# Performance work log

Hardware: AMD Instinct MI355X
Metric: run time of the kernel (lower is better)

The kernel has to match this reference:

```python
import jax, jax.numpy as jnp
import numpy as np

B, S, D, H = 4, 4096, 1024, 8
HD = D // H  # head dims, FFT length for circular convolution


def setup_inputs() -> dict:
    key = jax.random.key(0)
    k1, k2, k3 = jax.random.split(key, 3)
    x = jax.random.normal(k1, (B, S, D), dtype=jnp.float32)
    # torch nn.Linear(D, 3D, bias=False) -> store as [D, 3D] for x @ W
    w_qkv = jax.random.normal(k2, (D, 3 * D), dtype=jnp.float32) * (1.0 / np.sqrt(D))
    w_out = jax.random.normal(k3, (D, D), dtype=jnp.float32) * (1.0 / np.sqrt(D))
    return {"x": x, "w_qkv": w_qkv, "w_out": w_out}


def reference(x, w_qkv, w_out):
    # HRR self-attention (causal, norm=False, dropout in eval mode => identity).
    b, s, d = x.shape
    qkv = x @ w_qkv                               # [B,S,3D]
    q, k, v = jnp.split(qkv, 3, axis=-1)
    q = q.reshape(b, s, H, HD)
    k = k.reshape(b, s, H, HD)
    v = v.reshape(b, s, H, HD)
    # Holographic binding: circular convolution k (*) v == ifft(fft(k)*fft(v))
    fq = jnp.fft.fft(q, axis=-1)                  # [B,S,H,HD] complex
    fk = jnp.fft.fft(k, axis=-1)
    fv = jnp.fft.fft(v, axis=-1)
    kv = fk * fv                                  # bound key-value pairs (freq domain)
    kv = jnp.cumsum(kv, axis=1)                   # causal aggregation over sequence
    # Unbinding via circular correlation with the query: ifft(S * conj(fft(q)))
    vals = jnp.fft.ifft(kv * jnp.conj(fq), axis=-1).real.astype(x.dtype)
    vals = vals.reshape(b, s, d)
    return vals @ w_out
```

## Files before the change

### kernel.cpp

```cpp
#include <hip/hip_runtime.h>

static constexpr int BB = 4;
static constexpr int SS = 4096;
static constexpr int DD = 1024;
static constexpr int HH = 8;
static constexpr int HD = 128;
static constexpr int CS = 32;
static constexpr int NCHUNK = SS / CS;
static constexpr int MROWS = BB * SS;

typedef __attribute__((ext_vector_type(8))) short bfrag;
typedef __attribute__((ext_vector_type(4))) float floatx4;

__device__ __forceinline__ float bf2f(unsigned int u) {
    return __uint_as_float((u & 0xFFFFu) << 16);
}
__device__ __forceinline__ unsigned short f2bf(float f) {
    unsigned int x = __float_as_uint(f);
    unsigned int r = x + 0x7FFFu + ((x >> 16) & 1u);
    return (unsigned short)(r >> 16);
}
__device__ __forceinline__ unsigned int pack_rne(float a, float b) {
    return ((unsigned int)f2bf(a)) | (((unsigned int)f2bf(b)) << 16);
}

__device__ __forceinline__ void async_copy16(const void* g, void* l) {
    __builtin_amdgcn_global_load_lds(
        (const __attribute__((address_space(1))) unsigned int*)g,
        (__attribute__((address_space(3))) unsigned int*)l, 16, 0, 0);
}

struct cpx { float re, im; };

__device__ __forceinline__ cpx cadd(cpx a, cpx b) { return {a.re + b.re, a.im + b.im}; }
__device__ __forceinline__ cpx csub(cpx a, cpx b) { return {a.re - b.re, a.im - b.im}; }
__device__ __forceinline__ cpx cmul(cpx a, cpx b) {
    return { fmaf(a.re, b.re, -a.im * b.im), fmaf(a.re, b.im, a.im * b.re) };
}
__device__ __forceinline__ cpx cmul_cj(cpx a, cpx b) {
    return { fmaf(a.re, b.re, a.im * b.im), fmaf(a.im, b.re, -a.re * b.im) };
}
__device__ __forceinline__ cpx shflx(cpx x, int m) {
    return { __shfl_xor(x.re, m), __shfl_xor(x.im, m) };
}
__device__ __forceinline__ cpx shfl_at(cpx x, int src) {
    return { __shfl(x.re, src), __shfl(x.im, src) };
}

__device__ __forceinline__ int pair_lane_even(int l) {
    int m = (int)(__brev((unsigned)l) >> 26);
    int mp = (64 - m) & 63;
    return (int)(__brev((unsigned)mp) >> 26);
}

__device__ __forceinline__ void make_tw(int lane, cpx tw[7]) {
    const float NEG2PI = -6.28318530717958647692f;
    float a0 = NEG2PI * (float)lane * (1.0f / 128.0f);
    tw[0] = { __cosf(a0), __sinf(a0) };
    int d = 32;
#pragma unroll
    for (int s = 1; s <= 6; ++s) {
        int i = lane & (d - 1);
        float a = NEG2PI * (float)i / (float)(2 * d);
        tw[s] = { __cosf(a), __sinf(a) };
        d >>= 1;
    }
}

__device__ __forceinline__ void fft128_fwd(cpx& x0, cpx& x1, const cpx tw[7], int lane) {
    cpx a = x0, b = x1;
    x0 = cadd(a, b);
    x1 = cmul(csub(a, b), tw[0]);
    int d = 32;
#pragma unroll
    for (int s = 1; s <= 6; ++s) {
        const bool up = (lane & d) != 0;
        cpx o0 = shflx(x0, d);
        cpx o1 = shflx(x1, d);
        cpx s0 = cadd(x0, o0);
        cpx s1 = cadd(x1, o1);
        cpx d0 = cmul(csub(o0, x0), tw[s]);
        cpx d1 = cmul(csub(o1, x1), tw[s]);
        x0 = up ? d0 : s0;
        x1 = up ? d1 : s1;
        d >>= 1;
    }
}

__device__ __forceinline__ void fft128_inv(cpx& x0, cpx& x1, const cpx tw[7], int lane) {
    int d = 1;
#pragma unroll
    for (int s = 6; s >= 1; --s) {
        const bool up = (lane & d) != 0;
        cpx o0 = shflx(x0, d);
        cpx o1 = shflx(x1, d);
        cpx b0 = up ? x0 : o0;
        cpx a0 = up ? o0 : x0;
        cpx b1 = up ? x1 : o1;
        cpx a1 = up ? o1 : x1;
        cpx t0 = cmul_cj(b0, tw[s]);
        cpx t1 = cmul_cj(b1, tw[s]);
        x0 = up ? csub(a0, t0) : cadd(a0, t0);
        x1 = up ? csub(a1, t1) : cadd(a1, t1);
        d <<= 1;
    }
    cpx t = cmul_cj(x1, tw[0]);
    cpx a = x0;
    const float inv = 0.0078125f;
    x0 = { (a.re + t.re) * inv, (a.im + t.im) * inv };
    x1 = { (a.re - t.re) * inv, (a.im - t.im) * inv };
}

__global__ __launch_bounds__(256) void convert_bf16(const float* __restrict__ X,
                                                    unsigned short* __restrict__ Y)
{
    const size_t i = ((size_t)blockIdx.x * 256 + threadIdx.x) * 8;
    float4 v0 = *reinterpret_cast<const float4*>(X + i);
    float4 v1 = *reinterpret_cast<const float4*>(X + i + 4);
    uint4 p = { pack_rne(v0.x, v0.y), pack_rne(v0.z, v0.w),
                pack_rne(v1.x, v1.y), pack_rne(v1.z, v1.w) };
    *reinterpret_cast<uint4*>(Y + i) = p;
}

__global__ __launch_bounds__(256) void transpose_rn(const float* __restrict__ W,
                                                    unsigned short* __restrict__ T,
                                                    int K, int N)
{
    __shared__ float tile[32][33];
    const int n0 = blockIdx.x * 32, k0 = blockIdx.y * 32;
    const int r = threadIdx.x >> 5, c = threadIdx.x & 31;
#pragma unroll
    for (int i = 0; i < 4; ++i)
        tile[r + 8 * i][c] = W[(size_t)(k0 + r + 8 * i) * N + n0 + c];
    __syncthreads();
#pragma unroll
    for (int i = 0; i < 4; ++i) {
        float v = tile[c][r + 8 * i];
        T[(size_t)(n0 + r + 8 * i) * K + k0 + c] = f2bf(v);
    }
}

template <typename OutT>
__global__ __launch_bounds__(512, 2) void gemm256(const unsigned short* __restrict__ A,
                                                  const unsigned short* __restrict__ Bt,
                                                  OutT* __restrict__ C,
                                                  int M, int N, int K)
{
    extern __shared__ __align__(16) unsigned short lds[];
    unsigned short* sA = lds;
    unsigned short* sB = lds + 32768;

    const int tid = threadIdx.x, lane = tid & 63, w = tid >> 6;
    const int wr = w >> 2, wc = w & 3;

    const int nbx = N >> 8;
    const int cpx_ = gridDim.x >> 3;
    const int wg = blockIdx.x;
    const int swz = (wg & 7) * cpx_ + (wg >> 3);
    const int n0 = (swz % nbx) << 8;
    const int m0 = (swz / nbx) << 8;

    const int lr = lane >> 2;
    const int kx = (((lane & 3) ^ ((lane >> 3) & 3)) << 3);
    const unsigned short* pA0 = A  + (size_t)(m0 + 32 * w + lr) * K + kx;
    const unsigned short* pA1 = pA0 + (size_t)16 * K;
    const unsigned short* pB0 = Bt + (size_t)(n0 + 32 * w + lr) * K + kx;
    const unsigned short* pB1 = pB0 + (size_t)16 * K;

    auto stage = [&](int tt) {
        const int q = (tt & 3) * 8192;
        const size_t ko = (size_t)tt * 32;
        async_copy16(pA0 + ko, sA + q + (2 * w) * 512);
        async_copy16(pA1 + ko, sA + q + (2 * w + 1) * 512);
        async_copy16(pB0 + ko, sB + q + (2 * w) * 512);
        async_copy16(pB1 + ko, sB + q + (2 * w + 1) * 512);
    };

    const int sl = lane >> 4;
    const int xa = ((lane & 15) >> 1) & 3;
    const int ra = (wr * 128 + (lane & 15)) * 32 + ((sl ^ xa) << 3);
    const int rb = (wc * 64  + (lane & 15)) * 32 + ((sl ^ xa) << 3);

    floatx4 acc[8][4];
#pragma unroll
    for (int m = 0; m < 8; ++m)
#pragma unroll
        for (int n = 0; n < 4; ++n) { floatx4 z = {0.f, 0.f, 0.f, 0.f}; acc[m][n] = z; }

    const int NT = K >> 5;

    stage(0); stage(1); stage(2);

    for (int t = 0; t < NT; ++t) {
        if (t + 3 < NT) stage(t + 3);

        const int rem = NT - 1 - t;
        if (rem >= 3)      asm volatile("s_waitcnt vmcnt(12)" ::: "memory");
        else if (rem == 2) asm volatile("s_waitcnt vmcnt(8)"  ::: "memory");
        else if (rem == 1) asm volatile("s_waitcnt vmcnt(4)"  ::: "memory");
        else               asm volatile("s_waitcnt vmcnt(0)"  ::: "memory");
        __builtin_amdgcn_s_barrier();
        __builtin_amdgcn_sched_barrier(0);

        const unsigned short* pa = sA + (t & 3) * 8192 + ra;
        const unsigned short* pb = sB + (t & 3) * 8192 + rb;
        bfrag af[8], bfr[4];
#pragma unroll
        for (int m = 0; m < 8; ++m)
            af[m] = *reinterpret_cast<const bfrag*>(pa + m * 512);
#pragma unroll
        for (int n = 0; n < 4; ++n)
            bfr[n] = *reinterpret_cast<const bfrag*>(pb + n * 512);

        __builtin_amdgcn_s_setprio(1);
#pragma unroll
        for (int m = 0; m < 8; ++m)
#pragma unroll
            for (int n = 0; n < 4; ++n)
                acc[m][n] = __builtin_amdgcn_mfma_f32_16x16x32_bf16(af[m], bfr[n], acc[m][n], 0, 0, 0);
        __builtin_amdgcn_s_setprio(0);
        __builtin_amdgcn_sched_barrier(0);

        asm volatile("s_waitcnt lgkmcnt(0)" ::: "memory");
        __builtin_amdgcn_s_barrier();
        __builtin_amdgcn_sched_barrier(0);
    }

    if constexpr (sizeof(OutT) == 2) {
        unsigned short* myt = lds + w * 8192;
#pragma unroll
        for (int m = 0; m < 8; ++m)
#pragma unroll
            for (int n = 0; n < 4; ++n)
#pragma unroll
                for (int r = 0; r < 4; ++r)
                    myt[(m * 16 + sl * 4 + r) * 64 + n * 16 + (lane & 15)] = f2bf(acc[m][n][r]);
        asm volatile("s_waitcnt lgkmcnt(0)" ::: "memory");
#pragma unroll
        for (int c = 0; c < 16; ++c) {
            const int idx = c * 64 + lane;
            const int row = idx >> 3, cc = (idx & 7) << 3;
            uint4 v = *reinterpret_cast<const uint4*>(myt + idx * 8);
            *reinterpret_cast<uint4*>(C + (size_t)(m0 + wr * 128 + row) * N + (n0 + wc * 64 + cc)) = v;
        }
    } else {
#pragma unroll
        for (int m = 0; m < 8; ++m)
#pragma unroll
            for (int n = 0; n < 4; ++n)
#pragma unroll
                for (int r = 0; r < 4; ++r) {
                    const int row = m0 + wr * 128 + m * 16 + sl * 4 + r;
                    const int col = n0 + wc * 64 + n * 16 + (lane & 15);
                    C[(size_t)row * N + col] = acc[m][n][r];
                }
    }
}

__global__ __launch_bounds__(256) void hrr_phaseA(const unsigned short* __restrict__ qkv,
                                                  unsigned int* __restrict__ P,
                                                  float* __restrict__ totals)
{
    const int blk = blockIdx.x;
    const int bh = blk / NCHUNK;
    const int chunk = blk % NCHUNK;
    const int b = bh >> 3, h = bh & 7;
    const int tid = threadIdx.x;
    const int wave = tid >> 6, lane = tid & 63;

    cpx tw[7];
    make_tw(lane, tw);
    const int pl0 = pair_lane_even(lane);
    const int pl1 = lane ^ 63;

    cpx acc0 = {0.f, 0.f}, acc1 = {0.f, 0.f};
    const int s0 = chunk * CS + wave * (CS / 4);
    for (int i = 0; i < CS / 4; ++i) {
        const int s = s0 + i;
        const unsigned short* base = qkv + (size_t)(b * SS + s) * 3072 + h * 128;
        cpx z0 = { bf2f(base[1024 + lane]),      bf2f(base[2048 + lane]) };
        cpx z1 = { bf2f(base[1024 + 64 + lane]), bf2f(base[2048 + 64 + lane]) };
        fft128_fwd(z0, z1, tw, lane);
        cpx sq0 = cmul(z0, z0);
        cpx sq1 = cmul(z1, z1);
        cpx sp0 = shfl_at(sq0, pl0);
        cpx sp1 = shfl_at(sq1, pl1);
        cpx p0 = { 0.25f * (sq0.im + sp0.im), 0.25f * (sp0.re - sq0.re) };
        cpx p1 = { 0.25f * (sq1.im + sp1.im), 0.25f * (sp1.re - sq1.re) };
        acc0 = cadd(acc0, p0);
        acc1 = cadd(acc1, p1);
        unsigned int* prow = P + ((size_t)bh * SS + s) * 128;
        prow[lane]      = pack_rne(p0.re, p0.im);
        prow[64 + lane] = pack_rne(p1.re, p1.im);
    }

    __shared__ float red[4][256];
    red[wave][lane * 2 + 0] = acc0.re;
    red[wave][lane * 2 + 1] = acc0.im;
    red[wave][128 + lane * 2 + 0] = acc1.re;
    red[wave][128 + lane * 2 + 1] = acc1.im;
    __syncthreads();

    float s4 = red[0][tid] + red[1][tid] + red[2][tid] + red[3][tid];
    totals[((size_t)bh * NCHUNK + chunk) * 256 + tid] = s4;
}

__global__ __launch_bounds__(256) void hrr_phaseB(float* __restrict__ totals)
{
    const int bh = blockIdx.x;
    const int t = threadIdx.x;
    float run = 0.f;
#pragma unroll 4
    for (int c = 0; c < NCHUNK; ++c) {
        const size_t idx = ((size_t)bh * NCHUNK + c) * 256 + t;
        float v = totals[idx];
        totals[idx] = run;
        run += v;
    }
}

__global__ __launch_bounds__(256) void hrr_phaseC(const unsigned short* __restrict__ qkv,
                                                  const unsigned int* __restrict__ P,
                                                  const float* __restrict__ totals,
                                                  unsigned short* __restrict__ vals)
{
    __shared__ float Pf[CS * 256];

    const int blk = blockIdx.x;
    const int bh = blk / NCHUNK;
    const int chunk = blk % NCHUNK;
    const int b = bh >> 3, h = bh & 7;
    const int tid = threadIdx.x;
    const int wave = tid >> 6, lane = tid & 63;

    cpx tw[7];
    make_tw(lane, tw);
    const int pl0 = pair_lane_even(lane);
    const int pl1 = lane ^ 63;

#pragma unroll
    for (int it = 0; it < CS / 4; ++it) {
        const int sl = it * 4 + wave;
        const int s = chunk * CS + sl;
        const unsigned int* prow = P + ((size_t)bh * SS + s) * 128;
        unsigned int a = prow[lane];
        unsigned int c = prow[64 + lane];
        float2 fa = { bf2f(a), bf2f(a >> 16) };
        float2 fc = { bf2f(c), bf2f(c >> 16) };
        *reinterpret_cast<float2*>(&Pf[sl * 256 + 2 * lane]) = fa;
        *reinterpret_cast<float2*>(&Pf[sl * 256 + 128 + 2 * lane]) = fc;
    }
    __syncthreads();

    {
        float run = totals[((size_t)bh * NCHUNK + chunk) * 256 + tid];
#pragma unroll 8
        for (int s = 0; s < CS; ++s) {
            run += Pf[s * 256 + tid];
            Pf[s * 256 + tid] = run;
        }
    }
    __syncthreads();

    for (int i = 0; i < CS / 8; ++i) {
        const int sl = wave * (CS / 4) + 2 * i;
        const int s1 = chunk * CS + sl;
        const unsigned short* b1 = qkv + (size_t)(b * SS + s1) * 3072 + h * 128;
        const unsigned short* b2 = b1 + 3072;
        cpx z0 = { bf2f(b1[lane]),      bf2f(b2[lane]) };
        cpx z1 = { bf2f(b1[64 + lane]), bf2f(b2[64 + lane]) };
        fft128_fwd(z0, z1, tw, lane);
        cpx B0 = shfl_at(z0, pl0);
        cpx B1 = shfl_at(z1, pl1);
        cpx cf1_0 = { 0.5f * (z0.re + B0.re), 0.5f * (B0.im - z0.im) };
        cpx cf1_1 = { 0.5f * (z1.re + B1.re), 0.5f * (B1.im - z1.im) };
        cpx cf2_0 = { 0.5f * (z0.im + B0.im), 0.5f * (z0.re - B0.re) };
        cpx cf2_1 = { 0.5f * (z1.im + B1.im), 0.5f * (z1.re - B1.re) };

        const float* r1 = &Pf[sl * 256];
        const float* r2 = r1 + 256;
        float2 t0 = *reinterpret_cast<const float2*>(&r1[2 * lane]);
        float2 t1 = *reinterpret_cast<const float2*>(&r1[128 + 2 * lane]);
        float2 t2 = *reinterpret_cast<const float2*>(&r2[2 * lane]);
        float2 t3 = *reinterpret_cast<const float2*>(&r2[128 + 2 * lane]);
        cpx C1_0 = { t0.x, t0.y }, C1_1 = { t1.x, t1.y };
        cpx C2_0 = { t2.x, t2.y }, C2_1 = { t3.x, t3.y };

        cpx a0 = cmul(C1_0, cf1_0), w0 = cmul(C2_0, cf2_0);
        cpx a1 = cmul(C1_1, cf1_1), w1 = cmul(C2_1, cf2_1);
        cpx u0 = { a0.re - w0.im, a0.im + w0.re };
        cpx u1 = { a1.re - w1.im, a1.im + w1.re };
        fft128_inv(u0, u1, tw, lane);

        unsigned short* o1 = vals + (size_t)(b * SS + s1) * DD + h * 128;
        unsigned short* o2 = o1 + DD;
        o1[lane]      = f2bf(u0.re);
        o1[64 + lane] = f2bf(u1.re);
        o2[lane]      = f2bf(u0.im);
        o2[64 + lane] = f2bf(u1.im);
    }
}

extern "C" void kernel_launch(void* const* d_in, const int* in_sizes, int n_in,
                              void* d_out, int out_size, void* d_ws, size_t ws_size,
                              hipStream_t stream) {
    const float* x     = (const float*)d_in[0];
    const float* w_qkv = (const float*)d_in[1];
    const float* w_out = (const float*)d_in[2];
    float* out = (float*)d_out;

    unsigned short* qkv  = (unsigned short*)d_ws;
    unsigned short* xb   = qkv + (size_t)MROWS * 3072;
    unsigned short* vals = xb + (size_t)MROWS * DD;
    unsigned int* P      = (unsigned int*)(vals + (size_t)MROWS * DD);
    float* totals        = (float*)(P + (size_t)32 * SS * 128);
    unsigned short* wqkvt = (unsigned short*)(totals + (size_t)32 * NCHUNK * 256);
    unsigned short* woutt = wqkvt + (size_t)3072 * 1024;

    static bool attr_done = false;
    if (!attr_done) {
        hipFuncSetAttribute(reinterpret_cast<const void*>(gemm256<unsigned short>),
                            hipFuncAttributeMaxDynamicSharedMemorySize, 131072);
        hipFuncSetAttribute(reinterpret_cast<const void*>(gemm256<float>),
                            hipFuncAttributeMaxDynamicSharedMemorySize, 131072);
        attr_done = true;
    }

    convert_bf16<<<(MROWS * DD) / (256 * 8), 256, 0, stream>>>(x, xb);
    transpose_rn<<<dim3(3072 / 32, 1024 / 32), 256, 0, stream>>>(w_qkv, wqkvt, 1024, 3072);
    transpose_rn<<<dim3(1024 / 32, 1024 / 32), 256, 0, stream>>>(w_out, woutt, 1024, 1024);

    gemm256<unsigned short><<<(3072 / 256) * (MROWS / 256), 512, 131072, stream>>>(
        xb, wqkvt, qkv, MROWS, 3072, DD);

    hrr_phaseA<<<BB * HH * NCHUNK, 256, 0, stream>>>(qkv, P, totals);

    hrr_phaseB<<<BB * HH, 256, 0, stream>>>(totals);

    hrr_phaseC<<<BB * HH * NCHUNK, 256, 0, stream>>>(qkv, P, totals, vals);

    gemm256<float><<<(DD / 256) * (MROWS / 256), 512, 131072, stream>>>(
        vals, woutt, out, MROWS, DD, DD);
}
```

Baseline: 383.9 us.

## Restructure GEMM main loop into double-buffered 64-wide K tiles with interleaved staging

Replaces the 4-deep ring of 32-wide K stages with two 64-wide K buffers, each split into two 32-wide halves. Each iteration runs four MFMA sub-phases over half the M fragments, and issues async global-to-LDS copies for future tiles between them. The aim is to overlap memory loads with MFMA work more finely and to keep fewer fragment registers live per phase. In exchange there are more barriers per K step and hand-tuned vmcnt counts that must match the issue order exactly.

```diff
diff --git a/kernel.cpp b/kernel.cpp
--- a/kernel.cpp
+++ b/kernel.cpp
@@ -147,8 +147,6 @@
                                                   int M, int N, int K)
 {
     extern __shared__ __align__(16) unsigned short lds[];
-    unsigned short* sA = lds;
-    unsigned short* sB = lds + 32768;
 
     const int tid = threadIdx.x, lane = tid & 63, w = tid >> 6;
     const int wr = w >> 2, wc = w & 3;
@@ -162,24 +160,27 @@
 
     const int lr = lane >> 2;
     const int kx = (((lane & 3) ^ ((lane >> 3) & 3)) << 3);
-    const unsigned short* pA0 = A  + (size_t)(m0 + 32 * w + lr) * K + kx;
-    const unsigned short* pA1 = pA0 + (size_t)16 * K;
-    const unsigned short* pB0 = Bt + (size_t)(n0 + 32 * w + lr) * K + kx;
-    const unsigned short* pB1 = pB0 + (size_t)16 * K;
-
-    auto stage = [&](int tt) {
-        const int q = (tt & 3) * 8192;
-        const size_t ko = (size_t)tt * 32;
-        async_copy16(pA0 + ko, sA + q + (2 * w) * 512);
-        async_copy16(pA1 + ko, sA + q + (2 * w + 1) * 512);
-        async_copy16(pB0 + ko, sB + q + (2 * w) * 512);
-        async_copy16(pB1 + ko, sB + q + (2 * w + 1) * 512);
+    const unsigned short* gA = A  + (size_t)(m0 + 32 * w + lr) * K + kx;
+    const unsigned short* gB = Bt + (size_t)(n0 + 32 * w + lr) * K + kx;
+
+    auto stageA = [&](int buf, int kk, int kelem) {
+        unsigned short* dst = lds + buf * 32768 + kk * 8192 + (32 * w) * 32;
+        const unsigned short* src = gA + kelem;
+        async_copy16(src, dst);
+        async_copy16(src + (size_t)16 * K, dst + 512);
+    };
+    auto stageB = [&](int buf, int kk, int kelem) {
+        unsigned short* dst = lds + buf * 32768 + 16384 + kk * 8192 + (32 * w) * 32;
+        const unsigned short* src = gB + kelem;
+        async_copy16(src, dst);
+        async_copy16(src + (size_t)16 * K, dst + 512);
     };
 
     const int sl = lane >> 4;
     const int xa = ((lane & 15) >> 1) & 3;
-    const int ra = (wr * 128 + (lane & 15)) * 32 + ((sl ^ xa) << 3);
-    const int rb = (wc * 64  + (lane & 15)) * 32 + ((sl ^ xa) << 3);
+    const int soff = ((sl ^ xa) << 3);
+    const int ra = (wr * 128 + (lane & 15)) * 32 + soff;
+    const int rb = (wc * 64  + (lane & 15)) * 32 + soff;
 
     floatx4 acc[8][4];
 #pragma unroll
@@ -187,43 +188,107 @@
 #pragma unroll
         for (int n = 0; n < 4; ++n) { floatx4 z = {0.f, 0.f, 0.f, 0.f}; acc[m][n] = z; }
 
-    const int NT = K >> 5;
-
-    stage(0); stage(1); stage(2);
-
-    for (int t = 0; t < NT; ++t) {
-        if (t + 3 < NT) stage(t + 3);
-
-        const int rem = NT - 1 - t;
-        if (rem >= 3)      asm volatile("s_waitcnt vmcnt(12)" ::: "memory");
-        else if (rem == 2) asm volatile("s_waitcnt vmcnt(8)"  ::: "memory");
-        else if (rem == 1) asm volatile("s_waitcnt vmcnt(4)"  ::: "memory");
-        else               asm volatile("s_waitcnt vmcnt(0)"  ::: "memory");
-        __builtin_amdgcn_s_barrier();
-        __builtin_amdgcn_sched_barrier(0);
-
-        const unsigned short* pa = sA + (t & 3) * 8192 + ra;
-        const unsigned short* pb = sB + (t & 3) * 8192 + rb;
-        bfrag af[8], bfr[4];
-#pragma unroll
-        for (int m = 0; m < 8; ++m)
-            af[m] = *reinterpret_cast<const bfrag*>(pa + m * 512);
-#pragma unroll
-        for (int n = 0; n < 4; ++n)
-            bfr[n] = *reinterpret_cast<const bfrag*>(pb + n * 512);
-
-        __builtin_amdgcn_s_setprio(1);
-#pragma unroll
-        for (int m = 0; m < 8; ++m)
-#pragma unroll
-            for (int n = 0; n < 4; ++n)
-                acc[m][n] = __builtin_amdgcn_mfma_f32_16x16x32_bf16(af[m], bfr[n], acc[m][n], 0, 0, 0);
-        __builtin_amdgcn_s_setprio(0);
-        __builtin_amdgcn_sched_barrier(0);
-
-        asm volatile("s_waitcnt lgkmcnt(0)" ::: "memory");
-        __builtin_amdgcn_s_barrier();
-        __builtin_amdgcn_sched_barrier(0);
+    const int NT = K >> 6;
+
+    stageB(0, 0, 0);  stageA(0, 0, 0);
+    stageB(0, 1, 32); stageA(0, 1, 32);
+    stageB(1, 0, 64); stageA(1, 0, 64);
+    asm volatile("s_waitcnt vmcnt(8)" ::: "memory");
+    __builtin_amdgcn_s_barrier();
+
+    for (int i = 0; i < NT; ++i) {
+        const int bb = (i & 1) * 32768;
+        bfrag af0[4], af1[4], bf0[4], bf1[4];
+
+        {
+            const unsigned short* pA = lds + bb + ra;
+            const unsigned short* pB = lds + bb + 16384 + rb;
+#pragma unroll
+            for (int m = 0; m < 4; ++m) af0[m] = *reinterpret_cast<const bfrag*>(pA + m * 512);
+#pragma unroll
+            for (int n = 0; n < 4; ++n) bf0[n] = *reinterpret_cast<const bfrag*>(pB + n * 512);
+            if (i + 1 < NT) stageB((i + 1) & 1, 1, (i + 1) * 64 + 32);
+            __builtin_amdgcn_s_barrier();
+            asm volatile("s_waitcnt lgkmcnt(0)" ::: "memory");
+            __builtin_amdgcn_sched_barrier(0);
+            __builtin_amdgcn_s_setprio(1);
+#pragma unroll
+            for (int m = 0; m < 4; ++m)
+#pragma unroll
+                for (int n = 0; n < 4; ++n)
+                    acc[m][n] = __builtin_amdgcn_mfma_f32_16x16x32_bf16(af0[m], bf0[n], acc[m][n], 0, 0, 0);
+            __builtin_amdgcn_s_setprio(0);
+            __builtin_amdgcn_s_barrier();
+        }
+
+        {
+            const unsigned short* pA = lds + bb + ra + 2048;
+#pragma unroll
+            for (int m = 0; m < 4; ++m) af1[m] = *reinterpret_cast<const bfrag*>(pA + m * 512);
+            if (i + 1 < NT) {
+                stageA((i + 1) & 1, 1, (i + 1) * 64 + 32);
+                asm volatile("s_waitcnt vmcnt(6)" ::: "memory");
+            } else {
+                asm volatile("s_waitcnt vmcnt(0)" ::: "memory");
+            }
+            __builtin_amdgcn_s_barrier();
+            asm volatile("s_waitcnt lgkmcnt(0)" ::: "memory");
+            __builtin_amdgcn_sched_barrier(0);
+            __builtin_amdgcn_s_setprio(1);
+#pragma unroll
+            for (int m = 0; m < 4; ++m)
+#pragma unroll
+                for (int n = 0; n < 4; ++n)
+                    acc[4 + m][n] = __builtin_amdgcn_mfma_f32_16x16x32_bf16(af1[m], bf0[n], acc[4 + m][n], 0, 0, 0);
+            __builtin_amdgcn_s_setprio(0);
+            __builtin_amdgcn_s_barrier();
+        }
+
+        {
+            const unsigned short* pA = lds + bb + 8192 + ra;
+            const unsigned short* pB = lds + bb + 16384 + 8192 + rb;
+#pragma unroll
+            for (int m = 0; m < 4; ++m) af0[m] = *reinterpret_cast<const bfrag*>(pA + m * 512);
+#pragma unroll
+            for (int n = 0; n < 4; ++n) bf1[n] = *reinterpret_cast<const bfrag*>(pB + n * 512);
+            if (i + 2 < NT) stageB(i & 1, 0, (i + 2) * 64);
+            __builtin_amdgcn_s_barrier();
+            asm volatile("s_waitcnt lgkmcnt(0)" ::: "memory");
+            __builtin_amdgcn_sched_barrier(0);
+            __builtin_amdgcn_s_setprio(1);
+#pragma unroll
+            for (int m = 0; m < 4; ++m)
+#pragma unroll
+                for (int n = 0; n < 4; ++n)
+                    acc[m][n] = __builtin_amdgcn_mfma_f32_16x16x32_bf16(af0[m], bf1[n], acc[m][n], 0, 0, 0);
+            __builtin_amdgcn_s_setprio(0);
+            __builtin_amdgcn_s_barrier();
+        }
+
+        {
+            const unsigned short* pA = lds + bb + 8192 + ra + 2048;
+#pragma unroll
+            for (int m = 0; m < 4; ++m) af1[m] = *reinterpret_cast<const bfrag*>(pA + m * 512);
+            if (i + 2 < NT) {
+                stageA(i & 1, 0, (i + 2) * 64);
+                asm volatile("s_waitcnt vmcnt(6)" ::: "memory");
+            } else if (i + 1 < NT) {
+                asm volatile("s_waitcnt vmcnt(2)" ::: "memory");
+            } else {
+                asm volatile("s_waitcnt vmcnt(0)" ::: "memory");
+            }
+            __builtin_amdgcn_s_barrier();
+            asm volatile("s_waitcnt lgkmcnt(0)" ::: "memory");
+            __builtin_amdgcn_sched_barrier(0);
+            __builtin_amdgcn_s_setprio(1);
+#pragma unroll
+            for (int m = 0; m < 4; ++m)
+#pragma unroll
+                for (int n = 0; n < 4; ++n)
+                    acc[4 + m][n] = __builtin_amdgcn_mfma_f32_16x16x32_bf16(af1[m], bf1[n], acc[4 + m][n], 0, 0, 0);
+            __builtin_amdgcn_s_setprio(0);
+            __builtin_amdgcn_s_barrier();
+        }
     }
 
     if constexpr (sizeof(OutT) == 2) {
```

Result: faster. 371.3 us (-3.3%).
